# Performance work log

Measured on AMD Instinct MI355X. Metric: run time of the kernel, lower is better.

## Reference

```python
import jax, jax.numpy as jnp
import numpy as np

B, EMB, P, K = 8192, 768, 96, 256
D = EMB // P  # dsub = 8


def setup_inputs() -> dict:
    key = jax.random.key(0)
    k1, k2 = jax.random.split(key)
    vecs = jax.random.normal(k1, (B, EMB), dtype=jnp.float32)
    # torch init: uniform(-1, 1)
    codebook = jax.random.uniform(k2, (P, K, D), dtype=jnp.float32, minval=-1.0, maxval=1.0)
    return {"vecs": vecs, "codebook": codebook}


def reference(vecs, codebook):
    b = vecs.shape[0]
    p, k, d = codebook.shape
    v = vecs.reshape(b, p, d)                                  # [B,P,D]
    # squared distances via expanded quadratic (avoids [B,P,K,D] broadcast):
    # ||v-c||^2 = ||v||^2 - 2 v.c + ||c||^2
    dots = jnp.einsum('bpd,pkd->bpk', v, codebook)             # [B,P,K]
    d2 = (jnp.sum(v * v, axis=-1, keepdims=True)               # [B,P,1]
          - 2.0 * dots
          + jnp.sum(codebook * codebook, axis=-1)[None])       # [1,P,K]
    proba = jax.nn.softmax(-d2, axis=-1)                       # [B,P,K]
    # straight-through hard assignment
    idx = jnp.argmax(proba, axis=-1)                           # [B,P]
    hard = jax.nn.one_hot(idx, k, dtype=proba.dtype)           # [B,P,K]
    ste = jax.lax.stop_gradient(hard - proba) + proba
    # reconstruct from codebook
    out = jnp.einsum('bpk,pkd->bpd', ste, codebook).reshape(b, p * d)
    return out
```

## Files before the change

kernel.cpp:

```cpp
#include <hip/hip_runtime.h>


#define TPB 256
#define KBQ 2

namespace {
constexpr int kB   = 8192;
constexpr int kEMB = 768;
constexpr int kP   = 96;
constexpr int kK   = 256;
constexpr int kD   = 8;
}

__global__ __launch_bounds__(TPB, 6)
void pq_argmin_kernel(const float* __restrict__ vecs,
                      const float* __restrict__ codebook,
                      float* __restrict__ out)
{
    __shared__ alignas(16) float lds_code[kK][kD];
    __shared__ alignas(16) float lds_c2[kK];

    const int p = blockIdx.y;
    const int t = threadIdx.x;

    {
        const float4* cb4 =
            reinterpret_cast<const float4*>(codebook + (size_t)p * kK * kD);
        float4 a = cb4[2 * t];
        float4 b = cb4[2 * t + 1];
        float c2 = a.x * a.x + a.y * a.y + a.z * a.z + a.w * a.w +
                   b.x * b.x + b.y * b.y + b.z * b.z + b.w * b.w;
        float4* lc = reinterpret_cast<float4*>(&lds_code[t][0]);
        lc[0] = make_float4(-2.0f * a.x, -2.0f * a.y, -2.0f * a.z, -2.0f * a.w);
        lc[1] = make_float4(-2.0f * b.x, -2.0f * b.y, -2.0f * b.z, -2.0f * b.w);
        lds_c2[t] = c2;
    }
    __syncthreads();

    const int b0 = blockIdx.x * (TPB * KBQ) + t;

    float v[KBQ][kD];
#pragma unroll
    for (int q = 0; q < KBQ; ++q) {
        const float4* vp = reinterpret_cast<const float4*>(
            vecs + (size_t)(b0 + q * TPB) * kEMB + p * kD);
        float4 x = vp[0];
        float4 y = vp[1];
        v[q][0] = x.x; v[q][1] = x.y; v[q][2] = x.z; v[q][3] = x.w;
        v[q][4] = y.x; v[q][5] = y.y; v[q][6] = y.z; v[q][7] = y.w;
    }

    float best[KBQ];
    int   bidx[KBQ];
#pragma unroll
    for (int q = 0; q < KBQ; ++q) {
        best[q] = __builtin_inff();
        bidx[q] = 0;
    }

#pragma unroll 4
    for (int k = 0; k < kK; ++k) {
        const float4 c0  = *reinterpret_cast<const float4*>(&lds_code[k][0]);
        const float4 c1  = *reinterpret_cast<const float4*>(&lds_code[k][4]);
        const float  c2k = lds_c2[k];
#pragma unroll
        for (int q = 0; q < KBQ; ++q) {
            float s = fmaf(c0.x, v[q][0], c2k);
            s = fmaf(c0.y, v[q][1], s);
            s = fmaf(c0.z, v[q][2], s);
            s = fmaf(c0.w, v[q][3], s);
            s = fmaf(c1.x, v[q][4], s);
            s = fmaf(c1.y, v[q][5], s);
            s = fmaf(c1.z, v[q][6], s);
            s = fmaf(c1.w, v[q][7], s);
            if (s < best[q]) {
                best[q] = s;
                bidx[q] = k;
            }
        }
    }

#pragma unroll
    for (int q = 0; q < KBQ; ++q) {
        const float4* cr = reinterpret_cast<const float4*>(
            codebook + ((size_t)p * kK + bidx[q]) * kD);
        float4 r0 = cr[0];
        float4 r1 = cr[1];
        float4* op = reinterpret_cast<float4*>(
            out + (size_t)(b0 + q * TPB) * kEMB + p * kD);
        op[0] = r0;
        op[1] = r1;
    }
}

extern "C" void kernel_launch(void* const* d_in, const int* in_sizes, int n_in,
                              void* d_out, int out_size, void* d_ws, size_t ws_size,
                              hipStream_t stream)
{
    const float* vecs     = (const float*)d_in[0];
    const float* codebook = (const float*)d_in[1];
    float* out            = (float*)d_out;

    dim3 grid(kB / (TPB * KBQ), kP, 1);
    dim3 block(TPB, 1, 1);
    hipLaunchKernelGGL(pq_argmin_kernel, grid, block, 0, stream,
                       vecs, codebook, out);
}
```

Before: 120.0 us.

## Stream codebook through scalar loads into SGPRs instead of LDS reads

Each wave now reads codebook entries with s_load_dwordx16 into scalar registers, eight codes per chunk, and feeds them straight into the FMAs as scalar operands. This removes the per-iteration LDS vector reads of the codebook. The distance is rewritten as a maximisation of v·c − ½‖c‖², so only the half-norm stays in LDS. In exchange each chunk waits on lgkmcnt(0), which serialises scalar-load latency against compute unless occupancy hides it. It also puts heavy pressure on scalar registers (64 SGPRs per chunk).

```diff
diff --git a/kernel.cpp b/kernel.cpp
--- a/kernel.cpp
+++ b/kernel.cpp
@@ -3,6 +3,9 @@
 
 #define TPB 256
 #define KBQ 2
+#define CHUNK 8
+
+typedef float sf16 __attribute__((ext_vector_type(16)));
 
 namespace {
 constexpr int kB   = 8192;
@@ -12,13 +15,34 @@
 constexpr int kD   = 8;
 }
 
+template <int LO>
+__device__ __forceinline__ void pq_code(const sf16& blk, float h, int kk,
+                                        const float (&v)[KBQ][kD],
+                                        float (&best)[KBQ], int (&bidx)[KBQ])
+{
+#pragma unroll
+    for (int q = 0; q < KBQ; ++q) {
+        float g = fmaf(blk[LO + 0], v[q][0], h);
+        g = fmaf(blk[LO + 1], v[q][1], g);
+        g = fmaf(blk[LO + 2], v[q][2], g);
+        g = fmaf(blk[LO + 3], v[q][3], g);
+        g = fmaf(blk[LO + 4], v[q][4], g);
+        g = fmaf(blk[LO + 5], v[q][5], g);
+        g = fmaf(blk[LO + 6], v[q][6], g);
+        g = fmaf(blk[LO + 7], v[q][7], g);
+        if (g > best[q]) {
+            best[q] = g;
+            bidx[q] = kk;
+        }
+    }
+}
+
 __global__ __launch_bounds__(TPB, 6)
 void pq_argmin_kernel(const float* __restrict__ vecs,
                       const float* __restrict__ codebook,
                       float* __restrict__ out)
 {
-    __shared__ alignas(16) float lds_code[kK][kD];
-    __shared__ alignas(16) float lds_c2[kK];
+    __shared__ alignas(16) float lds_h[kK];
 
     const int p = blockIdx.y;
     const int t = threadIdx.x;
@@ -30,10 +54,7 @@
         float4 b = cb4[2 * t + 1];
         float c2 = a.x * a.x + a.y * a.y + a.z * a.z + a.w * a.w +
                    b.x * b.x + b.y * b.y + b.z * b.z + b.w * b.w;
-        float4* lc = reinterpret_cast<float4*>(&lds_code[t][0]);
-        lc[0] = make_float4(-2.0f * a.x, -2.0f * a.y, -2.0f * a.z, -2.0f * a.w);
-        lc[1] = make_float4(-2.0f * b.x, -2.0f * b.y, -2.0f * b.z, -2.0f * b.w);
-        lds_c2[t] = c2;
+        lds_h[t] = -0.5f * c2;
     }
     __syncthreads();
 
@@ -54,30 +75,38 @@
     int   bidx[KBQ];
 #pragma unroll
     for (int q = 0; q < KBQ; ++q) {
-        best[q] = __builtin_inff();
+        best[q] = -__builtin_inff();
         bidx[q] = 0;
     }
 
-#pragma unroll 4
-    for (int k = 0; k < kK; ++k) {
-        const float4 c0  = *reinterpret_cast<const float4*>(&lds_code[k][0]);
-        const float4 c1  = *reinterpret_cast<const float4*>(&lds_code[k][4]);
-        const float  c2k = lds_c2[k];
-#pragma unroll
-        for (int q = 0; q < KBQ; ++q) {
-            float s = fmaf(c0.x, v[q][0], c2k);
-            s = fmaf(c0.y, v[q][1], s);
-            s = fmaf(c0.z, v[q][2], s);
-            s = fmaf(c0.w, v[q][3], s);
-            s = fmaf(c1.x, v[q][4], s);
-            s = fmaf(c1.y, v[q][5], s);
-            s = fmaf(c1.z, v[q][6], s);
-            s = fmaf(c1.w, v[q][7], s);
-            if (s < best[q]) {
-                best[q] = s;
-                bidx[q] = k;
-            }
-        }
+    const float* cbp = codebook + (size_t)p * kK * kD;
+
+    for (int c = 0; c < kK / CHUNK; ++c) {
+        sf16 sA, sB, sC, sD;
+        asm volatile("s_load_dwordx16 %0, %1, 0x0"  : "=s"(sA) : "s"(cbp));
+        asm volatile("s_load_dwordx16 %0, %1, 0x40" : "=s"(sB) : "s"(cbp));
+        asm volatile("s_load_dwordx16 %0, %1, 0x80" : "=s"(sC) : "s"(cbp));
+        asm volatile("s_load_dwordx16 %0, %1, 0xc0" : "=s"(sD) : "s"(cbp));
+
+        const float4 h0 = *reinterpret_cast<const float4*>(&lds_h[c * CHUNK]);
+        const float4 h1 = *reinterpret_cast<const float4*>(&lds_h[c * CHUNK + 4]);
+        const float hh[CHUNK] = {h0.x, h0.y, h0.z, h0.w,
+                                 h1.x, h1.y, h1.z, h1.w};
+
+        asm volatile("s_waitcnt lgkmcnt(0)" ::: "memory");
+        __builtin_amdgcn_sched_barrier(0);
+
+        const int kbase = c * CHUNK;
+        pq_code<0>(sA, hh[0], kbase + 0, v, best, bidx);
+        pq_code<8>(sA, hh[1], kbase + 1, v, best, bidx);
+        pq_code<0>(sB, hh[2], kbase + 2, v, best, bidx);
+        pq_code<8>(sB, hh[3], kbase + 3, v, best, bidx);
+        pq_code<0>(sC, hh[4], kbase + 4, v, best, bidx);
+        pq_code<8>(sC, hh[5], kbase + 5, v, best, bidx);
+        pq_code<0>(sD, hh[6], kbase + 6, v, best, bidx);
+        pq_code<8>(sD, hh[7], kbase + 7, v, best, bidx);
+
+        cbp += CHUNK * kD;
     }
 
 #pragma unroll
```

Result: slower. 139.0 us (+15.8%).
